# Optimization experiments

Hardware: AMD Instinct MI355X
Metric: run time of the kernel (lower is better)

Reference implementation:

```python
import jax, jax.numpy as jnp
import numpy as np

ALPHA = 0.2
NEG = -9e15
EPS = 1e-5


def _gat(h, adj, W, a, out_features):
    # h: [B,N,Fin], adj: [B,N,N], W: [Fin,Fout], a: [2*Fout,1]
    Wh = jnp.matmul(h, W)                      # [B,N,Fout]
    Wh1 = jnp.matmul(Wh, a[:out_features])     # [B,N,1]
    Wh2 = jnp.matmul(Wh, a[out_features:])     # [B,N,1]
    e = Wh1 + jnp.swapaxes(Wh2, 1, 2)          # [B,N,N]
    e = jax.nn.leaky_relu(e, negative_slope=ALPHA)
    scores = jnp.where(adj > 0, e, NEG)
    att = jax.nn.softmax(scores, axis=1)       # NOTE: dim=1 as in source
    return jnp.matmul(att, Wh)                 # [B,N,Fout]


def _layernorm(x, g, b):
    mu = jnp.mean(x, axis=-1, keepdims=True)
    var = jnp.var(x, axis=-1, keepdims=True)
    return (x - mu) * jax.lax.rsqrt(var + EPS) * g + b


def setup_inputs() -> dict:
    key = jax.random.key(0)
    ks = jax.random.split(key, 8)
    B, N, F, H = 2, 4096, 256, 1024
    x = jax.random.normal(ks[0], (B, N, F), dtype=jnp.float32)
    adj = jax.random.randint(ks[1], (B, N, N), 0, 2, dtype=jnp.int32)
    def xavier(k, shape):
        fan_in, fan_out = shape[0], shape[1]
        lim = np.sqrt(6.0 / (fan_in + fan_out))
        return jax.random.uniform(k, shape, jnp.float32, -lim, lim)
    return {
        "x": x,
        "adj": adj,
        "W1": xavier(ks[2], (F, F)),
        "a1": xavier(ks[3], (2 * F, 1)),
        "W2": xavier(ks[4], (F, F)),
        "a2": xavier(ks[5], (2 * F, 1)),
        "w_ff1": xavier(ks[6], (F, H)) ,
        "b_ff1": jnp.zeros((H,), jnp.float32),
        "w_ff2": xavier(ks[7], (H, F)),
        "b_ff2": jnp.zeros((F,), jnp.float32),
        "g_ln1": jnp.ones((F,), jnp.float32),
        "b_ln1": jnp.zeros((F,), jnp.float32),
        "g_ln2": jnp.ones((F,), jnp.float32),
        "b_ln2": jnp.zeros((F,), jnp.float32),
    }


def reference(x, adj, W1, a1, W2, a2, w_ff1, b_ff1, w_ff2, b_ff2,
              g_ln1, b_ln1, g_ln2, b_ln2):
    Fout = W1.shape[1]
    residual = x
    # dropout is a no-op in eval mode
    h = _gat(x, adj, W1, a1, Fout)          # single head -> cat is identity
    h = _gat(h, adj, W2, a2, W2.shape[1])
    h = _layernorm(residual + h, g_ln1, b_ln1)
    residual2 = h
    ff = jnp.matmul(jax.nn.relu(jnp.matmul(h, w_ff1) + b_ff1), w_ff2) + b_ff2
    return _layernorm(residual2 + ff, g_ln2, b_ln2)
```

## Files before the change

### kernel.cpp

```cpp
#include <hip/hip_runtime.h>
#include <math.h>

#define ALPHA 0.2f
#define NEGV  -9e15f
#define EPSV  1e-5f

constexpr int B_ = 2, N_ = 4096, F_ = 256, H_ = 1024;
constexpr int SPLIT_ = 16;
constexpr int SPLITJ_ = 4;

typedef __attribute__((ext_vector_type(4))) float f32x4;
typedef __attribute__((ext_vector_type(8))) short s16x8;

__device__ __forceinline__ unsigned short f2bf(float f) {
    unsigned u = __builtin_bit_cast(unsigned, f);
    u += 0x7fffu + ((u >> 16) & 1u);
    return (unsigned short)(u >> 16);
}

__global__ __launch_bounds__(256) void transp_all_kernel(
    const float* __restrict__ W1, const float* __restrict__ W2,
    const float* __restrict__ F1s, const float* __restrict__ F2s,
    unsigned short* __restrict__ D1, unsigned short* __restrict__ D2,
    unsigned short* __restrict__ D3, unsigned short* __restrict__ D4,
    float* __restrict__ Zp)
{
    const int mi = blockIdx.z;
    const float* src; unsigned short* dst; int R, Cc;
    if (mi == 0)      { src = W1;  dst = D1; R = 256;  Cc = 256; }
    else if (mi == 1) { src = W2;  dst = D2; R = 256;  Cc = 256; }
    else if (mi == 2) { src = F1s; dst = D3; R = 256;  Cc = 1024; }
    else              { src = F2s; dst = D4; R = 1024; Cc = 256; }
    const int r0 = blockIdx.x * 64, c0 = blockIdx.y * 64;
    const int t = threadIdx.x;

    if (mi == 0 && blockIdx.y >= 4) {
        const int lid = (blockIdx.y - 4) * 16 + blockIdx.x;
        if (lid < 32) {
            const int i = (lid * 256 + t) * 4;
            *(float4*)&Zp[i] = make_float4(0.f, 0.f, 0.f, 0.f);
        }
        return;
    }
    if (r0 >= R || c0 >= Cc) return;

    __shared__ float T[64][65];
    #pragma unroll
    for (int s = 0; s < 4; ++s) {
        const int rr = s * 16 + (t >> 4);
        const int cq = t & 15;
        const float4 v = *(const float4*)&src[(size_t)(r0 + rr) * Cc + c0 + cq * 4];
        T[rr][cq * 4 + 0] = v.x; T[rr][cq * 4 + 1] = v.y;
        T[rr][cq * 4 + 2] = v.z; T[rr][cq * 4 + 3] = v.w;
    }
    __syncthreads();
    #pragma unroll
    for (int s = 0; s < 4; ++s) {
        const int cr = s * 16 + (t >> 4);
        const int rq = t & 15;
        ushort4 o;
        o.x = f2bf(T[rq * 4 + 0][cr]);
        o.y = f2bf(T[rq * 4 + 1][cr]);
        o.z = f2bf(T[rq * 4 + 2][cr]);
        o.w = f2bf(T[rq * 4 + 3][cr]);
        *(ushort4*)&dst[(size_t)(c0 + cr) * R + r0 + rq * 4] = o;
    }
}

__global__ __launch_bounds__(256) void gemm128_kernel(
    const void* __restrict__ Ap, const unsigned short* __restrict__ Wt,
    const float* __restrict__ bias, void* __restrict__ Cp,
    unsigned short* __restrict__ Tout, const float* __restrict__ wha,
    float* __restrict__ Wh1, float* __restrict__ Wh2,
    int Nc, int K, int relu, int a_bf16, int c_mode)
{
    __shared__ unsigned short As[128 * 72];
    __shared__ unsigned short Bs[128 * 72];
    const int t = threadIdx.x;
    const int w = t >> 6, l = t & 63;
    const int quad = l >> 4, l15 = l & 15;
    const int wr = w & 1, wc = w >> 1;
    const int row0 = blockIdx.y * 128, col0 = blockIdx.x * 128;
    const int sr = t >> 1;
    const int sk = (t & 1) * 32;

    f32x4 acc[4][4];
    #pragma unroll
    for (int it = 0; it < 4; ++it)
        #pragma unroll
        for (int ft = 0; ft < 4; ++ft) acc[it][ft] = (f32x4)(0.f);

    for (int k0 = 0; k0 < K; k0 += 64) {
        if (a_bf16) {
            const unsigned short* ap =
                (const unsigned short*)Ap + (size_t)(row0 + sr) * K + k0 + sk;
            #pragma unroll
            for (int u = 0; u < 4; ++u)
                *(s16x8*)&As[sr * 72 + sk + u * 8] = *(const s16x8*)(ap + u * 8);
        } else {
            const float* ap = (const float*)Ap + (size_t)(row0 + sr) * K + k0 + sk;
            #pragma unroll
            for (int u = 0; u < 8; ++u) {
                const float4 v = *(const float4*)(ap + u * 4);
                ushort4 o;
                o.x = f2bf(v.x); o.y = f2bf(v.y); o.z = f2bf(v.z); o.w = f2bf(v.w);
                *(ushort4*)&As[sr * 72 + sk + u * 4] = o;
            }
        }
        {
            const unsigned short* bp = Wt + (size_t)(col0 + sr) * K + k0 + sk;
            #pragma unroll
            for (int u = 0; u < 4; ++u)
                *(s16x8*)&Bs[sr * 72 + sk + u * 8] = *(const s16x8*)(bp + u * 8);
        }
        __syncthreads();
        #pragma unroll
        for (int ks = 0; ks < 64; ks += 32) {
            s16x8 af[4], bf[4];
            #pragma unroll
            for (int it = 0; it < 4; ++it)
                af[it] = *(const s16x8*)&As[(wr * 64 + it * 16 + l15) * 72 + ks + quad * 8];
            #pragma unroll
            for (int ft = 0; ft < 4; ++ft)
                bf[ft] = *(const s16x8*)&Bs[(wc * 64 + ft * 16 + l15) * 72 + ks + quad * 8];
            #pragma unroll
            for (int ft = 0; ft < 4; ++ft)
                #pragma unroll
                for (int it = 0; it < 4; ++it)
                    acc[it][ft] = __builtin_amdgcn_mfma_f32_16x16x32_bf16(
                        af[it], bf[ft], acc[it][ft], 0, 0, 0);
        }
        __syncthreads();
    }

    if (c_mode) {
        #pragma unroll
        for (int ft = 0; ft < 4; ++ft) {
            const int col = col0 + wc * 64 + ft * 16 + l15;
            const float bv = bias ? bias[col] : 0.f;
            #pragma unroll
            for (int it = 0; it < 4; ++it) {
                const int rbase = row0 + wr * 64 + it * 16 + quad * 4;
                #pragma unroll
                for (int rr = 0; rr < 4; ++rr) {
                    float v = acc[it][ft][rr] + bv;
                    if (relu) v = fmaxf(v, 0.f);
                    if (c_mode == 2)
                        ((unsigned short*)Cp)[(size_t)(rbase + rr) * Nc + col] = f2bf(v);
                    else
                        ((float*)Cp)[(size_t)(rbase + rr) * Nc + col] = v;
                }
            }
        }
    }

    if (Tout) {
        const int bb = row0 >> 12;
        #pragma unroll
        for (int ft = 0; ft < 4; ++ft) {
            const int col = col0 + wc * 64 + ft * 16 + l15;
            #pragma unroll
            for (int it = 0; it < 4; ++it) {
                const int ibase = (row0 & (N_ - 1)) + wr * 64 + it * 16 + quad * 4;
                ushort4 o;
                o.x = f2bf(acc[it][ft][0]); o.y = f2bf(acc[it][ft][1]);
                o.z = f2bf(acc[it][ft][2]); o.w = f2bf(acc[it][ft][3]);
                *(ushort4*)&Tout[((size_t)bb * F_ + col) * N_ + ibase] = o;
            }
        }
    }

    if (wha) {
        float a1v[4], a2v[4];
        #pragma unroll
        for (int ft = 0; ft < 4; ++ft) {
            const int col = col0 + wc * 64 + ft * 16 + l15;
            a1v[ft] = wha[col];
            a2v[ft] = wha[F_ + col];
        }
        #pragma unroll
        for (int it = 0; it < 4; ++it)
            #pragma unroll
            for (int rr = 0; rr < 4; ++rr) {
                float s1 = 0.f, s2 = 0.f;
                #pragma unroll
                for (int ft = 0; ft < 4; ++ft) {
                    s1 += acc[it][ft][rr] * a1v[ft];
                    s2 += acc[it][ft][rr] * a2v[ft];
                }
                #pragma unroll
                for (int mkk = 1; mkk < 16; mkk <<= 1) {
                    s1 += __shfl_xor(s1, mkk);
                    s2 += __shfl_xor(s2, mkk);
                }
                if (l15 == 0) {
                    const int row = row0 + wr * 64 + it * 16 + quad * 4 + rr;
                    atomicAdd(&Wh1[row], s1);
                    atomicAdd(&Wh2[row], s2);
                }
            }
    }
}

__global__ __launch_bounds__(256) void gemm32_kernel(
    const void* __restrict__ Ap, const unsigned short* __restrict__ Wt,
    const float* __restrict__ bias, void* __restrict__ Cp,
    unsigned short* __restrict__ Tout, const float* __restrict__ wha,
    float* __restrict__ Wh1, float* __restrict__ Wh2,
    int Nc, int K, int relu, int a_mode, int c_mode)
{
    __shared__ unsigned short As[32 * 72];
    __shared__ unsigned short Bs[128 * 72];
    const int t = threadIdx.x;
    const int w = t >> 6, l = t & 63;
    const int quad = l >> 4, l15 = l & 15;
    const int row0 = blockIdx.y * 32, col0 = blockIdx.x * 128;
    const int sra = t >> 3;
    const int ska = (t & 7) * 8;
    const int srb = t >> 1;
    const int skb = (t & 1) * 32;

    f32x4 acc[2][2];
    #pragma unroll
    for (int it = 0; it < 2; ++it)
        #pragma unroll
        for (int ft = 0; ft < 2; ++ft) acc[it][ft] = (f32x4)(0.f);

    for (int k0 = 0; k0 < K; k0 += 64) {
        if (a_mode == 1) {
            const unsigned short* ap =
                (const unsigned short*)Ap + (size_t)(row0 + sra) * K + k0 + ska;
            *(s16x8*)&As[sra * 72 + ska] = *(const s16x8*)ap;
        } else if (a_mode == 0) {
            const float* ap = (const float*)Ap + (size_t)(row0 + sra) * K + k0 + ska;
            #pragma unroll
            for (int u = 0; u < 2; ++u) {
                const float4 v = *(const float4*)(ap + u * 4);
                ushort4 o;
                o.x = f2bf(v.x); o.y = f2bf(v.y); o.z = f2bf(v.z); o.w = f2bf(v.w);
                *(ushort4*)&As[sra * 72 + ska + u * 4] = o;
            }
        } else {
            const size_t S = (size_t)B_ * N_ * F_;
            const float* ap = (const float*)Ap + (size_t)(row0 + sra) * K + k0 + ska;
            #pragma unroll
            for (int u = 0; u < 2; ++u) {
                const float4 a = *(const float4*)(ap + u * 4);
                const float4 b = *(const float4*)(ap + S + u * 4);
                const float4 c = *(const float4*)(ap + 2 * S + u * 4);
                const float4 d = *(const float4*)(ap + 3 * S + u * 4);
                ushort4 o;
                o.x = f2bf(a.x + b.x + c.x + d.x);
                o.y = f2bf(a.y + b.y + c.y + d.y);
                o.z = f2bf(a.z + b.z + c.z + d.z);
                o.w = f2bf(a.w + b.w + c.w + d.w);
                *(ushort4*)&As[sra * 72 + ska + u * 4] = o;
            }
        }
        {
            const unsigned short* bp = Wt + (size_t)(col0 + srb) * K + k0 + skb;
            #pragma unroll
            for (int u = 0; u < 4; ++u)
                *(s16x8*)&Bs[srb * 72 + skb + u * 8] = *(const s16x8*)(bp + u * 8);
        }
        __syncthreads();
        #pragma unroll
        for (int ks = 0; ks < 64; ks += 32) {
            s16x8 af[2], bf[2];
            #pragma unroll
            for (int it = 0; it < 2; ++it)
                af[it] = *(const s16x8*)&As[(it * 16 + l15) * 72 + ks + quad * 8];
            #pragma unroll
            for (int ft = 0; ft < 2; ++ft)
                bf[ft] = *(const s16x8*)&Bs[(w * 32 + ft * 16 + l15) * 72 + ks + quad * 8];
            #pragma unroll
            for (int ft = 0; ft < 2; ++ft)
                #pragma unroll
                for (int it = 0; it < 2; ++it)
                    acc[it][ft] = __builtin_amdgcn_mfma_f32_16x16x32_bf16(
                        af[it], bf[ft], acc[it][ft], 0, 0, 0);
        }
        __syncthreads();
    }

    if (c_mode) {
        #pragma unroll
        for (int ft = 0; ft < 2; ++ft) {
            const int col = col0 + w * 32 + ft * 16 + l15;
            const float bv = bias ? bias[col] : 0.f;
            #pragma unroll
            for (int it = 0; it < 2; ++it) {
                const int rbase = row0 + it * 16 + quad * 4;
                #pragma unroll
                for (int rr = 0; rr < 4; ++rr) {
                    float v = acc[it][ft][rr] + bv;
                    if (relu) v = fmaxf(v, 0.f);
                    if (c_mode == 2)
                        ((unsigned short*)Cp)[(size_t)(rbase + rr) * Nc + col] = f2bf(v);
                    else
                        ((float*)Cp)[(size_t)(rbase + rr) * Nc + col] = v;
                }
            }
        }
    }

    if (Tout) {
        const int bb = row0 >> 12;
        #pragma unroll
        for (int ft = 0; ft < 2; ++ft) {
            const int col = col0 + w * 32 + ft * 16 + l15;
            #pragma unroll
            for (int it = 0; it < 2; ++it) {
                const int ibase = (row0 & (N_ - 1)) + it * 16 + quad * 4;
                ushort4 o;
                o.x = f2bf(acc[it][ft][0]); o.y = f2bf(acc[it][ft][1]);
                o.z = f2bf(acc[it][ft][2]); o.w = f2bf(acc[it][ft][3]);
                *(ushort4*)&Tout[((size_t)bb * F_ + col) * N_ + ibase] = o;
            }
        }
    }

    if (wha) {
        float a1v[2], a2v[2];
        #pragma unroll
        for (int ft = 0; ft < 2; ++ft) {
            const int col = col0 + w * 32 + ft * 16 + l15;
            a1v[ft] = wha[col];
            a2v[ft] = wha[F_ + col];
        }
        #pragma unroll
        for (int it = 0; it < 2; ++it)
            #pragma unroll
            for (int rr = 0; rr < 4; ++rr) {
                float s1 = acc[it][0][rr] * a1v[0] + acc[it][1][rr] * a1v[1];
                float s2 = acc[it][0][rr] * a2v[0] + acc[it][1][rr] * a2v[1];
                #pragma unroll
                for (int mkk = 1; mkk < 16; mkk <<= 1) {
                    s1 += __shfl_xor(s1, mkk);
                    s2 += __shfl_xor(s2, mkk);
                }
                if (l15 == 0) {
                    const int row = row0 + it * 16 + quad * 4 + rr;
                    atomicAdd(&Wh1[row], s1);
                    atomicAdd(&Wh2[row], s2);
                }
            }
    }
}

__global__ __launch_bounds__(256) void colstats_adj_kernel(
    const int* __restrict__ adj, unsigned long long* __restrict__ maskOut,
    const float* __restrict__ Wh1, const float* __restrict__ Wh2,
    float* __restrict__ pM, float* __restrict__ pS)
{
    const int t = threadIdx.x;
    const int j = blockIdx.x * 256 + t;
    const int sp = blockIdx.y;
    const int b = blockIdx.z;
    const int i0 = sp * (N_ / SPLIT_);
    const int w = t >> 6, l = t & 63;
    const float w2 = Wh2[b * N_ + j];
    const float* __restrict__ w1p = Wh1 + b * N_ + i0;
    const int* __restrict__ ap = adj + ((size_t)b * N_ + i0) * N_ + j;

    float m = -3.4e38f, s = 0.f;
    for (int c = 0; c < N_ / SPLIT_; c += 8) {
        int v[8];
        #pragma unroll
        for (int u = 0; u < 8; ++u) v[u] = ap[(size_t)(c + u) * N_];
        float x[8];
        #pragma unroll
        for (int u = 0; u < 8; ++u) {
            const bool act = v[u] > 0;
            const unsigned long long bm = __ballot(act);
            if (l == 0)
                maskOut[((size_t)b * N_ + i0 + c + u) * (N_ / 64) + blockIdx.x * 4 + w] = bm;
            const float e0 = w1p[c + u] + w2;
            const float e = fmaxf(e0, ALPHA * e0);
            x[u] = act ? e : NEGV;
        }
        const float cm = fmaxf(fmaxf(fmaxf(x[0], x[1]), fmaxf(x[2], x[3])),
                               fmaxf(fmaxf(x[4], x[5]), fmaxf(x[6], x[7])));
        const float nm = fmaxf(m, cm);
        float cs = 0.f;
        #pragma unroll
        for (int u = 0; u < 8; ++u) cs += __expf(x[u] - nm);
        s = s * __expf(m - nm) + cs;
        m = nm;
    }
    pM[((size_t)b * SPLIT_ + sp) * N_ + j] = m;
    pS[((size_t)b * SPLIT_ + sp) * N_ + j] = s;
}

__global__ __launch_bounds__(256) void colstats3_kernel(
    const unsigned long long* __restrict__ mask,
    const float* __restrict__ Wh1, const float* __restrict__ Wh2,
    float* __restrict__ pM, float* __restrict__ pS)
{
    const int t = threadIdx.x;
    const int j = blockIdx.x * 256 + t;
    const int sp = blockIdx.y;
    const int b = blockIdx.z;
    const int i0 = sp * (N_ / SPLIT_);
    const int w = t >> 6;
    const int jbit = t & 63;
    const float w2 = Wh2[b * N_ + j];
    const unsigned long long* __restrict__ mbase =
        mask + ((size_t)b * N_ + i0) * (N_ / 64) + blockIdx.x * 4 + w;
    const float* __restrict__ w1p = Wh1 + b * N_ + i0;

    float m = -3.4e38f, s = 0.f;
    for (int c = 0; c < N_ / SPLIT_; c += 8) {
        float x[8];
        #pragma unroll
        for (int u = 0; u < 8; ++u) {
            const unsigned long long mw = mbase[(size_t)(c + u) * (N_ / 64)];
            const float e0 = w1p[c + u] + w2;
            const float e = fmaxf(e0, ALPHA * e0);
            x[u] = ((mw >> jbit) & 1ull) ? e : NEGV;
        }
        const float cm = fmaxf(fmaxf(fmaxf(x[0], x[1]), fmaxf(x[2], x[3])),
                               fmaxf(fmaxf(x[4], x[5]), fmaxf(x[6], x[7])));
        const float nm = fmaxf(m, cm);
        float cs = 0.f;
        #pragma unroll
        for (int u = 0; u < 8; ++u) cs += __expf(x[u] - nm);
        s = s * __expf(m - nm) + cs;
        m = nm;
    }
    pM[((size_t)b * SPLIT_ + sp) * N_ + j] = m;
    pS[((size_t)b * SPLIT_ + sp) * N_ + j] = s;
}

__global__ __launch_bounds__(256) void colfin2_kernel(
    const float* __restrict__ pM, const float* __restrict__ pS,
    float* __restrict__ Mo)
{
    const int j = blockIdx.x * 256 + threadIdx.x;
    const int b = blockIdx.y;
    float m = -3.4e38f;
    #pragma unroll
    for (int s = 0; s < SPLIT_; ++s)
        m = fmaxf(m, pM[((size_t)b * SPLIT_ + s) * N_ + j]);
    float sum = 0.f;
    #pragma unroll
    for (int s = 0; s < SPLIT_; ++s)
        sum += pS[((size_t)b * SPLIT_ + s) * N_ + j] *
               __expf(pM[((size_t)b * SPLIT_ + s) * N_ + j] - m);
    Mo[b * N_ + j] = m + logf(sum);
}

__global__ __launch_bounds__(512, 4) void att_mfma8_kernel(
    const unsigned short* __restrict__ mask16, const unsigned short* __restrict__ Wht,
    const float* __restrict__ Wh1, const float* __restrict__ Wh2,
    const float* __restrict__ Mo, float* __restrict__ part)
{
    __shared__ unsigned short Ps[2][64 * 72];
    __shared__ float w2s[1024];
    __shared__ float mos[1024];

    const int t = threadIdx.x;
    const int w = t >> 6, l = t & 63;
    const int quad = l >> 4, l15 = l & 15;
    const int itg = w & 1;
    const int ftg = w >> 1;

    const int lin = blockIdx.x + (blockIdx.y << 6) + (blockIdx.z << 8);
    const int xcd = lin & 7;
    const int b = xcd >> 2;
    const int sp = xcd & 3;
    const int i0 = (lin >> 3) << 6;
    const int jbase = sp * (N_ / SPLITJ_);

    const int pi = t >> 3;
    const int pj8 = t & 7;
    const float w1i = Wh1[b * N_ + i0 + pi];
    const unsigned short* __restrict__ mrow =
        mask16 + ((size_t)b * N_ + i0 + pi) * (N_ / 16);
    const unsigned short* __restrict__ WhtB = Wht + (size_t)b * F_ * N_;

    if (t < 256) {
        const float4 a = *(const float4*)&Wh2[b * N_ + jbase + t * 4];
        const float4 c = *(const float4*)&Mo[b * N_ + jbase + t * 4];
        *(float4*)&w2s[t * 4] = a;
        *(float4*)&mos[t * 4] = c;
    }

    f32x4 acc[2][4];
    #pragma unroll
    for (int it = 0; it < 2; ++it)
        #pragma unroll
        for (int ft = 0; ft < 4; ++ft) acc[it][ft] = (f32x4)(0.f);

    const unsigned short* __restrict__ bbase =
        WhtB + (size_t)(ftg * 64 + l15) * N_ + jbase + quad * 8;

    s16x8 bA[8], bB[8];

    auto prefB = [&](int itr2, s16x8* dst) {
        const unsigned short* nb = bbase + itr2 * 64;
        #pragma unroll
        for (int ft = 0; ft < 4; ++ft)
            #pragma unroll
            for (int kk = 0; kk < 2; ++kk)
                dst[ft * 2 + kk] = *(const s16x8*)&nb[(size_t)ft * 16 * N_ + kk * 32];
    };

    auto computeP = [&](int itr2, unsigned short* psdst) {
        const unsigned mword = mrow[(jbase >> 4) + itr2 * 4 + (pj8 >> 1)];
        const unsigned mb = (mword >> ((pj8 & 1) * 8)) & 0xffu;
        const int jl = itr2 * 64 + pj8 * 8;
        s16x8 o;
        #pragma unroll
        for (int u4 = 0; u4 < 2; ++u4) {
            const float4 w2v = *(const float4*)&w2s[jl + u4 * 4];
            const float4 mov = *(const float4*)&mos[jl + u4 * 4];
            #pragma unroll
            for (int u = 0; u < 4; ++u) {
                const float xw = w1i + (&w2v.x)[u];
                const float e = fmaxf(xw, ALPHA * xw);
                const float x2 = ((mb >> (u4 * 4 + u)) & 1u) ? e : NEGV;
                o[u4 * 4 + u] = (short)f2bf(__expf(x2 - (&mov.x)[u]));
            }
        }
        *(s16x8*)&psdst[pi * 72 + pj8 * 8] = o;
    };

    auto mfmaStep = [&](const unsigned short* ps, const s16x8* breg) {
        #pragma unroll
        for (int ksidx = 0; ksidx < 2; ++ksidx) {
            s16x8 af[2];
            #pragma unroll
            for (int it = 0; it < 2; ++it)
                af[it] = *(const s16x8*)&ps[(itg * 32 + it * 16 + l15) * 72 +
                                            ksidx * 32 + quad * 8];
            #pragma unroll
            for (int ft = 0; ft < 4; ++ft)
                #pragma unroll
                for (int it = 0; it < 2; ++it)
                    acc[it][ft] = __builtin_amdgcn_mfma_f32_16x16x32_bf16(
                        af[it], breg[ft * 2 + ksidx], acc[it][ft], 0, 0, 0);
        }
    };

    prefB(0, bA);
    __syncthreads();
    computeP(0, &Ps[0][0]);
    __syncthreads();

    constexpr int NITER = (N_ / SPLITJ_) / 64;
    for (int itr = 0; itr < NITER; itr += 2) {
        prefB(itr + 1, bB);
        computeP(itr + 1, &Ps[1][0]);
        mfmaStep(&Ps[0][0], bA);
        __syncthreads();
        if (itr + 2 < NITER) {
            prefB(itr + 2, bA);
            computeP(itr + 2, &Ps[0][0]);
        }
        mfmaStep(&Ps[1][0], bB);
        __syncthreads();
    }

    float* __restrict__ pout = part + ((size_t)sp * B_ + b) * N_ * F_;
    #pragma unroll
    for (int it = 0; it < 2; ++it)
        #pragma unroll
        for (int ft = 0; ft < 4; ++ft) {
            const int col = ftg * 64 + ft * 16 + l15;
            #pragma unroll
            for (int rr = 0; rr < 4; ++rr) {
                const int row = i0 + itg * 32 + it * 16 + quad * 4 + rr;
                pout[(size_t)row * F_ + col] = acc[it][ft][rr];
            }
        }
}

__global__ __launch_bounds__(256) void addln4_kernel(
    const float* __restrict__ X, const float* __restrict__ p,
    const float* __restrict__ g, const float* __restrict__ bta,
    float* __restrict__ outf, unsigned short* __restrict__ outb)
{
    const int row = blockIdx.x;
    const int t = threadIdx.x;
    const size_t idx = (size_t)row * F_ + t;
    const size_t S = (size_t)B_ * N_ * F_;
    const float v = X[idx] + p[idx] + p[idx + S] + p[idx + 2 * S] + p[idx + 3 * S];
    float s1 = v, s2 = v * v;
    #pragma unroll
    for (int off = 32; off > 0; off >>= 1) {
        s1 += __shfl_down(s1, off);
        s2 += __shfl_down(s2, off);
    }
    __shared__ float r1[4], r2[4];
    __shared__ float mu_s, rs_s;
    const int wid = t >> 6, lane = t & 63;
    if (lane == 0) { r1[wid] = s1; r2[wid] = s2; }
    __syncthreads();
    if (t == 0) {
        const float a = r1[0] + r1[1] + r1[2] + r1[3];
        const float q = r2[0] + r2[1] + r2[2] + r2[3];
        const float mu = a * (1.f / F_);
        const float var = q * (1.f / F_) - mu * mu;
        mu_s = mu;
        rs_s = rsqrtf(var + EPSV);
    }
    __syncthreads();
    const float r = (v - mu_s) * rs_s * g[t] + bta[t];
    outf[idx] = r;
    outb[idx] = f2bf(r);
}

__global__ __launch_bounds__(256) void addln_kernel(
    const float* __restrict__ X, const float* __restrict__ Y,
    const float* __restrict__ g, const float* __restrict__ bta,
    float* __restrict__ out)
{
    const int row = blockIdx.x;
    const int t = threadIdx.x;
    const size_t idx = (size_t)row * F_ + t;
    const float v = X[idx] + Y[idx];
    float s1 = v, s2 = v * v;
    #pragma unroll
    for (int off = 32; off > 0; off >>= 1) {
        s1 += __shfl_down(s1, off);
        s2 += __shfl_down(s2, off);
    }
    __shared__ float r1[4], r2[4];
    __shared__ float mu_s, rs_s;
    const int wid = t >> 6, lane = t & 63;
    if (lane == 0) { r1[wid] = s1; r2[wid] = s2; }
    __syncthreads();
    if (t == 0) {
        const float a = r1[0] + r1[1] + r1[2] + r1[3];
        const float q = r2[0] + r2[1] + r2[2] + r2[3];
        const float mu = a * (1.f / F_);
        const float var = q * (1.f / F_) - mu * mu;
        mu_s = mu;
        rs_s = rsqrtf(var + EPSV);
    }
    __syncthreads();
    out[idx] = (v - mu_s) * rs_s * g[t] + bta[t];
}

extern "C" void kernel_launch(void* const* d_in, const int* in_sizes, int n_in,
                              void* d_out, int out_size, void* d_ws, size_t ws_size,
                              hipStream_t stream)
{
    const float* x     = (const float*)d_in[0];
    const int*   adj   = (const int*)d_in[1];
    const float* W1    = (const float*)d_in[2];
    const float* a1    = (const float*)d_in[3];
    const float* W2    = (const float*)d_in[4];
    const float* a2    = (const float*)d_in[5];
    const float* w_ff1 = (const float*)d_in[6];
    const float* b_ff1 = (const float*)d_in[7];
    const float* w_ff2 = (const float*)d_in[8];
    const float* b_ff2 = (const float*)d_in[9];
    const float* g_ln1 = (const float*)d_in[10];
    const float* b_ln1 = (const float*)d_in[11];
    const float* g_ln2 = (const float*)d_in[12];
    const float* b_ln2 = (const float*)d_in[13];
    float* out = (float*)d_out;

    const int Rtot = B_ * N_;
    char* wsb = (char*)d_ws;
    float* part  = (float*)wsb;
    float* ln1   = (float*)(wsb + 33554432);
    float* ffout = (float*)(wsb + 41943040);
    unsigned short* mid  = (unsigned short*)(wsb + 50331648);
    unsigned short* ln1b = (unsigned short*)(wsb + 67108864);
    unsigned short* Wht  = (unsigned short*)(wsb + 75497472);
    unsigned long long* mask = (unsigned long long*)(wsb + 79691776);
    unsigned short* mask16 = (unsigned short*)mask;
    unsigned short* Wt1  = (unsigned short*)(wsb + 83886080);
    unsigned short* Wt2  = Wt1 + 65536;
    unsigned short* Wtf1 = Wt2 + 65536;
    unsigned short* Wtf2 = Wtf1 + 262144;
    float* WhA1 = (float*)(wsb + 85196800);
    float* WhA2 = WhA1 + 8192;
    float* WhB1 = WhA2 + 8192;
    float* WhB2 = WhB1 + 8192;
    float* Mo   = (float*)(wsb + 85327872);
    float* pM   = (float*)(wsb + 85360640);
    float* pS   = (float*)(wsb + 85884928);

    const dim3 statsG(N_ / 256, SPLIT_, B_);
    const dim3 finG(N_ / 256, B_);
    const dim3 attG(N_ / 64, SPLITJ_, B_);

    transp_all_kernel<<<dim3(16, 16, 4), 256, 0, stream>>>(
        W1, W2, w_ff1, w_ff2, Wt1, Wt2, Wtf1, Wtf2, WhA1);

    gemm32_kernel<<<dim3(2, 256), 256, 0, stream>>>(
        x, Wt1, nullptr, nullptr, Wht, a1, WhA1, WhA2, F_, F_, 0, 0, 0);
    colstats_adj_kernel<<<statsG, 256, 0, stream>>>(adj, mask, WhA1, WhA2, pM, pS);
    colfin2_kernel<<<finG, 256, 0, stream>>>(pM, pS, Mo);
    att_mfma8_kernel<<<attG, 512, 0, stream>>>(mask16, Wht, WhA1, WhA2, Mo, part);

    gemm32_kernel<<<dim3(2, 256), 256, 0, stream>>>(
        part, Wt2, nullptr, nullptr, Wht, a2, WhB1, WhB2, F_, F_, 0, 2, 0);
    colstats3_kernel<<<statsG, 256, 0, stream>>>(mask, WhB1, WhB2, pM, pS);
    colfin2_kernel<<<finG, 256, 0, stream>>>(pM, pS, Mo);
    att_mfma8_kernel<<<attG, 512, 0, stream>>>(mask16, Wht, WhB1, WhB2, Mo, part);

    addln4_kernel<<<Rtot, 256, 0, stream>>>(x, part, g_ln1, b_ln1, ln1, ln1b);

    gemm128_kernel<<<dim3(8, 64), 256, 0, stream>>>(
        ln1b, Wtf1, b_ff1, mid, nullptr, nullptr, nullptr, nullptr, H_, F_, 1, 1, 2);
    gemm32_kernel<<<dim3(2, 256), 256, 0, stream>>>(
        mid, Wtf2, b_ff2, ffout, nullptr, nullptr, nullptr, nullptr, F_, H_, 0, 1, 1);

    addln_kernel<<<Rtot, 256, 0, stream>>>(ln1, ffout, g_ln2, b_ln2, out);
}
```

Baseline: 472.7 us.

## Fuse column softmax finalization into attention kernel and single-buffer B operands

Removes the separate colfin2 kernel: each attention block now reduces the per-split max/sum partials for its own 1024 columns into shared memory before the main loop. This saves two kernel launches and the Mo round trip, at the cost of redundant reduction work repeated across blocks sharing the same columns. The main loop is also restructured to a single B register buffer with a one-step loop, with the prefetch issued after the MFMA step. This lowers register pressure but hides less global-load latency.

```diff
diff --git a/kernel.cpp b/kernel.cpp
--- a/kernel.cpp
+++ b/kernel.cpp
@@ -432,28 +432,11 @@
     pS[((size_t)b * SPLIT_ + sp) * N_ + j] = s;
 }
 
-__global__ __launch_bounds__(256) void colfin2_kernel(
-    const float* __restrict__ pM, const float* __restrict__ pS,
-    float* __restrict__ Mo)
-{
-    const int j = blockIdx.x * 256 + threadIdx.x;
-    const int b = blockIdx.y;
-    float m = -3.4e38f;
-    #pragma unroll
-    for (int s = 0; s < SPLIT_; ++s)
-        m = fmaxf(m, pM[((size_t)b * SPLIT_ + s) * N_ + j]);
-    float sum = 0.f;
-    #pragma unroll
-    for (int s = 0; s < SPLIT_; ++s)
-        sum += pS[((size_t)b * SPLIT_ + s) * N_ + j] *
-               __expf(pM[((size_t)b * SPLIT_ + s) * N_ + j] - m);
-    Mo[b * N_ + j] = m + logf(sum);
-}
-
-__global__ __launch_bounds__(512, 4) void att_mfma8_kernel(
+__global__ __launch_bounds__(512, 4) void att_mfma9_kernel(
     const unsigned short* __restrict__ mask16, const unsigned short* __restrict__ Wht,
     const float* __restrict__ Wh1, const float* __restrict__ Wh2,
-    const float* __restrict__ Mo, float* __restrict__ part)
+    const float* __restrict__ pM, const float* __restrict__ pS,
+    float* __restrict__ part)
 {
     __shared__ unsigned short Ps[2][64 * 72];
     __shared__ float w2s[1024];
@@ -481,9 +464,24 @@
 
     if (t < 256) {
         const float4 a = *(const float4*)&Wh2[b * N_ + jbase + t * 4];
-        const float4 c = *(const float4*)&Mo[b * N_ + jbase + t * 4];
         *(float4*)&w2s[t * 4] = a;
-        *(float4*)&mos[t * 4] = c;
+    }
+    {
+        #pragma unroll
+        for (int jj = 0; jj < 2; ++jj) {
+            const int jl = t + jj * 512;
+            const int j = jbase + jl;
+            float m = -3.4e38f;
+            #pragma unroll
+            for (int s = 0; s < SPLIT_; ++s)
+                m = fmaxf(m, pM[((size_t)b * SPLIT_ + s) * N_ + j]);
+            float sum = 0.f;
+            #pragma unroll
+            for (int s = 0; s < SPLIT_; ++s)
+                sum += pS[((size_t)b * SPLIT_ + s) * N_ + j] *
+                       __expf(pM[((size_t)b * SPLIT_ + s) * N_ + j] - m);
+            mos[jl] = m + logf(sum);
+        }
     }
 
     f32x4 acc[2][4];
@@ -495,15 +493,15 @@
     const unsigned short* __restrict__ bbase =
         WhtB + (size_t)(ftg * 64 + l15) * N_ + jbase + quad * 8;
 
-    s16x8 bA[8], bB[8];
-
-    auto prefB = [&](int itr2, s16x8* dst) {
+    s16x8 bA[8];
+
+    auto prefB = [&](int itr2) {
         const unsigned short* nb = bbase + itr2 * 64;
         #pragma unroll
         for (int ft = 0; ft < 4; ++ft)
             #pragma unroll
             for (int kk = 0; kk < 2; ++kk)
-                dst[ft * 2 + kk] = *(const s16x8*)&nb[(size_t)ft * 16 * N_ + kk * 32];
+                bA[ft * 2 + kk] = *(const s16x8*)&nb[(size_t)ft * 16 * N_ + kk * 32];
     };
 
     auto computeP = [&](int itr2, unsigned short* psdst) {
@@ -526,7 +524,7 @@
         *(s16x8*)&psdst[pi * 72 + pj8 * 8] = o;
     };
 
-    auto mfmaStep = [&](const unsigned short* ps, const s16x8* breg) {
+    auto mfmaStep = [&](const unsigned short* ps) {
         #pragma unroll
         for (int ksidx = 0; ksidx < 2; ++ksidx) {
             s16x8 af[2];
@@ -539,26 +537,21 @@
                 #pragma unroll
                 for (int it = 0; it < 2; ++it)
                     acc[it][ft] = __builtin_amdgcn_mfma_f32_16x16x32_bf16(
-                        af[it], breg[ft * 2 + ksidx], acc[it][ft], 0, 0, 0);
+                        af[it], bA[ft * 2 + ksidx], acc[it][ft], 0, 0, 0);
         }
     };
 
-    prefB(0, bA);
+    prefB(0);
     __syncthreads();
     computeP(0, &Ps[0][0]);
     __syncthreads();
 
     constexpr int NITER = (N_ / SPLITJ_) / 64;
-    for (int itr = 0; itr < NITER; itr += 2) {
-        prefB(itr + 1, bB);
-        computeP(itr + 1, &Ps[1][0]);
-        mfmaStep(&Ps[0][0], bA);
-        __syncthreads();
-        if (itr + 2 < NITER) {
-            prefB(itr + 2, bA);
-            computeP(itr + 2, &Ps[0][0]);
-        }
-        mfmaStep(&Ps[1][0], bB);
+    for (int itr = 0; itr < NITER; ++itr) {
+        const int cur = itr & 1;
+        if (itr + 1 < NITER) computeP(itr + 1, &Ps[cur ^ 1][0]);
+        mfmaStep(&Ps[cur][0]);
+        if (itr + 1 < NITER) prefB(itr + 1);
         __syncthreads();
     }
 
@@ -681,12 +674,10 @@
     float* WhA2 = WhA1 + 8192;
     float* WhB1 = WhA2 + 8192;
     float* WhB2 = WhB1 + 8192;
-    float* Mo   = (float*)(wsb + 85327872);
     float* pM   = (float*)(wsb + 85360640);
     float* pS   = (float*)(wsb + 85884928);
 
     const dim3 statsG(N_ / 256, SPLIT_, B_);
-    const dim3 finG(N_ / 256, B_);
     const dim3 attG(N_ / 64, SPLITJ_, B_);
 
     transp_all_kernel<<<dim3(16, 16, 4), 256, 0, stream>>>(
@@ -695,14 +686,12 @@
     gemm32_kernel<<<dim3(2, 256), 256, 0, stream>>>(
         x, Wt1, nullptr, nullptr, Wht, a1, WhA1, WhA2, F_, F_, 0, 0, 0);
     colstats_adj_kernel<<<statsG, 256, 0, stream>>>(adj, mask, WhA1, WhA2, pM, pS);
-    colfin2_kernel<<<finG, 256, 0, stream>>>(pM, pS, Mo);
-    att_mfma8_kernel<<<attG, 512, 0, stream>>>(mask16, Wht, WhA1, WhA2, Mo, part);
+    att_mfma9_kernel<<<attG, 512, 0, stream>>>(mask16, Wht, WhA1, WhA2, pM, pS, part);
 
     gemm32_kernel<<<dim3(2, 256), 256, 0, stream>>>(
         part, Wt2, nullptr, nullptr, Wht, a2, WhB1, WhB2, F_, F_, 0, 2, 0);
     colstats3_kernel<<<statsG, 256, 0, stream>>>(mask, WhB1, WhB2, pM, pS);
-    colfin2_kernel<<<finG, 256, 0, stream>>>(pM, pS, Mo);
-    att_mfma8_kernel<<<attG, 512, 0, stream>>>(mask16, Wht, WhB1, WhB2, Mo, part);
+    att_mfma9_kernel<<<attG, 512, 0, stream>>>(mask16, Wht, WhB1, WhB2, pM, pS, part);
 
     addln4_kernel<<<Rtot, 256, 0, stream>>>(x, part, g_ln1, b_ln1, ln1, ln1b);
 
```

New measurement: 472.8 us. Within noise of the previous version (+0.0%).
